# Performance work log

Measured on AMD Instinct MI355X. Metric: run time of the kernel, lower is better.

The kernel has to match this reference:

```python
import jax, jax.numpy as jnp
import numpy as np

N_RF = 25   # contour integration RF extent (must be odd, 7-55)
N_CH = 96   # AlexNet conv1 feature maps


def _get_coaligned_masks(weights_type, rf_len, non_overlapping_rfs=True):
    """Faithful numpy replication of the manually-defined coalignment masks."""
    half_rf = rf_len // 2
    kernel = np.zeros((N_CH, rf_len, rf_len), dtype=np.float32)
    step = 3 if non_overlapping_rfs else 1
    pre = list(range(0, half_rf, step))
    post = list(range(half_rf + step, rf_len, step))
    kernel[10, pre, half_rf] = 1
    kernel[10, post, half_rf] = 1
    if weights_type != 'enhance':
        kernel[10, half_rf, pre] = -1
        kernel[10, half_rf, post] = -1
    kernel[5, half_rf, pre] = 1
    kernel[5, half_rf, post] = 1
    if weights_type != 'enhance':
        kernel[5, pre, half_rf] = -1
        kernel[5, post, half_rf] = -1
    kernel[54, (1, 4, 6, 9, 15, 17, 20, 23), (8, 9, 10, 11, 13, 14, 15, 16)] = 1
    kernel[64, list(range(0, half_rf, 3)), list(range(0, half_rf, 3))] = 1
    kernel[64, list(range(half_rf + 3, rf_len, 3)), list(range(half_rf + 3, rf_len, 3))] = 1
    if weights_type != 'enhance':
        kernel[64, list(range(rf_len - 1, half_rf, -3)), list(range(0, half_rf, 3))] = -1
        kernel[64, list(range(half_rf - 3, -1, -3)), list(range(half_rf + 3, rf_len, 3))] = -1
    kernel[67, :, :] = np.copy(kernel[54, :, :])
    kernel[78, (1, 3, 7, 10, 14, 17, 21, 23), (17, 16, 14, 13, 11, 10, 8, 7)] = 1
    return kernel


def setup_inputs() -> dict:
    key = jax.random.key(0)
    x = jax.random.normal(key, (128, 55, 55, N_CH), dtype=jnp.float32)  # NHWC, AlexNet conv1 output
    kernel = jnp.asarray(_get_coaligned_masks('enhance_and_suppress', N_RF))  # [ch, n, n]
    return {"x": x, "kernel": kernel}


def reference(x, kernel):
    # The per-(i,j) python loop in the original is exactly a per-channel (depthwise)
    # cross-correlation with the fixed mask kernel, SAME padding (n//2 each side),
    # followed by (identity) activation and residual add.
    ch = x.shape[-1]
    k = jnp.transpose(kernel, (1, 2, 0))[:, :, None, :]  # [n, n, 1, ch] HWIO depthwise
    lateral = jax.lax.conv_general_dilated(
        x, k,
        window_strides=(1, 1),
        padding='SAME',
        dimension_numbers=('NHWC', 'HWIO', 'NHWC'),
        feature_group_count=ch,
    )
    # activation is linear (None) -> identity
    return lateral + x
```

## Files before the change

### kernel.cpp

```cpp
#include <hip/hip_runtime.h>

#define NCH   96
#define RF    25
#define HALF  12
#define HW    55
#define PLANE (HW * HW)
#define CAP   32
#define MAXA  4
#define NGRP  12

#define WS_META_OFF (NCH * 4 + NCH * CAP * 4 * 2)

__global__ __launch_bounds__(1024) void prep_all(
        const float* __restrict__ kern, int* __restrict__ counts,
        int* __restrict__ tap_off, float* __restrict__ tap_w,
        int* __restrict__ meta) {
    __shared__ int scnt[NCH];
    const int wave = threadIdx.x >> 6;
    const int lane = threadIdx.x & 63;
    for (int c = wave; c < NCH; c += 16) {
        const float* kc = kern + c * (RF * RF);
        int base = 0;
        for (int seg = 0; seg < RF * RF; seg += 64) {
            const int i = seg + lane;
            const float w = (i < RF * RF) ? kc[i] : 0.0f;
            const unsigned long long m = __ballot(w != 0.0f);
            const int pos = base + __popcll(m & ((1ull << lane) - 1ull));
            if (w != 0.0f && pos < CAP) {
                const int dy = i / RF, dx = i - dy * RF;
                tap_off[c * CAP + pos] = (dy << 8) | dx;
                tap_w[c * CAP + pos]   = w;
            }
            base += __popcll(m);
        }
        if (lane == 0) { counts[c] = base; scnt[c] = base; }
    }
    __syncthreads();
    if (threadIdx.x == 0) {
        int na[2] = {0, 0};
        bool fallback = false;
        for (int ch = 0; ch < NCH; ++ch) {
            if (scnt[ch] > 0) {
                if (scnt[ch] > CAP) fallback = true;
                const int h = ch / 48;
                if (na[h] < MAXA) meta[3 + h * MAXA + na[h]] = ch;
                ++na[h];
            }
        }
        if (na[0] > MAXA || na[1] > MAXA) fallback = true;
        meta[0] = fallback ? 999 : 0;
        meta[1] = na[0] < MAXA ? na[0] : MAXA;
        meta[2] = na[1] < MAXA ? na[1] : MAXA;
        for (int h = 0; h < 2; ++h)
            for (int i = na[h]; i < MAXA; ++i) meta[3 + h * MAXA + i] = 0;
    }
}

__global__ __launch_bounds__(1024, 4) void contour_img(
        const float* __restrict__ x, const float* __restrict__ kern,
        const int* __restrict__ counts, const int* __restrict__ tap_off,
        const float* __restrict__ tap_w, const int* __restrict__ meta,
        float* __restrict__ out) {
    __shared__ float sh[MAXA][HW][56];
    __shared__ float lat[MAXA * PLANE];
    __shared__ float tw[MAXA][CAP];
    __shared__ int   toff[MAXA][CAP];
    __shared__ int   tcnt[MAXA];
    __shared__ signed char c2l[48];
    __shared__ int   wrNow[NGRP];
    __shared__ int   dsec[3];
    __shared__ int   ndsS;

    const int tid = threadIdx.x;
    const int b   = blockIdx.x;
    const int n   = b >> 1;
    const int h   = b & 1;

    const float* xn = x   + (size_t)n * (PLANE * NCH);
    float*       on = out + (size_t)n * (PLANE * NCH);

    const bool fast = (meta[0] != 999);
    const int  na   = fast ? meta[1 + h] : 0;

    if (tid < 48) c2l[tid] = -1;
    __syncthreads();
    if (fast) {
        if (tid < na) {
            const int c = meta[3 + h * MAXA + tid];
            tcnt[tid] = counts[c];
            c2l[c - h * 48] = (signed char)tid;
        }
        if (tid >= 64 && tid < 64 + MAXA * CAP) {
            const int a = (tid - 64) / CAP, t = (tid - 64) % CAP;
            const int c = (a < na) ? meta[3 + h * MAXA + a] : h * 48;
            toff[a][t] = tap_off[c * CAP + t];
            tw[a][t]   = tap_w[c * CAP + t];
        }
    }
    __syncthreads();
    if (fast && tid == 0) {
        int nds = 0;
        for (int s = 0; s < 3; ++s) {
            bool act = false;
            for (int c = s * 16; c < s * 16 + 16; ++c) act |= (c2l[c] >= 0);
            for (int g = s * 4; g < s * 4 + 4; ++g) wrNow[g] = act ? 0 : 1;
            if (act) dsec[nds++] = s;
        }
        ndsS = nds;
    }
    __syncthreads();

    if (fast) {
        const float4* xs = (const float4*)xn;
        float4*       os = (float4*)on;
        const int base = h * NGRP;

        #pragma unroll 2
        for (int idx = tid; idx < PLANE * NGRP; idx += 1024) {
            const int px = idx / NGRP;
            const int gg = idx - px * NGRP;
            const int fi = px * 24 + base + gg;
            const float4 v = xs[fi];
            const int r = px / HW, col = px - r * HW;
            const int lc = gg * 4;
            const int a0 = c2l[lc + 0], a1 = c2l[lc + 1];
            const int a2 = c2l[lc + 2], a3 = c2l[lc + 3];
            if (a0 >= 0) sh[a0][r][col] = v.x;
            if (a1 >= 0) sh[a1][r][col] = v.y;
            if (a2 >= 0) sh[a2][r][col] = v.z;
            if (a3 >= 0) sh[a3][r][col] = v.w;
            if (wrNow[gg]) os[fi] = v;
        }
        __syncthreads();

        for (int idx = tid; idx < na * PLANE; idx += 1024) {
            const int a = idx / PLANE, p = idx - a * PLANE;
            const int r = p / HW, col = p - r * HW;
            const int cnt = tcnt[a];
            float acc = 0.0f;
            for (int t = 0; t < cnt; ++t) {
                const int off = toff[a][t];
                const float w = tw[a][t];
                const int yy = r   + (off >> 8)  - HALF;
                const int xx = col + (off & 255) - HALF;
                const bool ok = ((unsigned)yy < (unsigned)HW) &
                                ((unsigned)xx < (unsigned)HW);
                const int yc = min(max(yy, 0), HW - 1);
                const int xc = min(max(xx, 0), HW - 1);
                const float vv = sh[a][yc][xc];
                acc += ok ? w * vv : 0.0f;
            }
            lat[idx] = acc;
        }
        __syncthreads();

        const int nds  = ndsS;
        const int tot2 = PLANE * nds * 4;
        for (int idx = tid; idx < tot2; idx += 1024) {
            const int px  = idx / (nds * 4);
            const int rem = idx - px * (nds * 4);
            const int d = rem >> 2, j = rem & 3;
            const int gg = dsec[d] * 4 + j;
            const int fi = px * 24 + base + gg;
            float4 v = xs[fi];
            const int lc = gg * 4;
            const int a0 = c2l[lc + 0], a1 = c2l[lc + 1];
            const int a2 = c2l[lc + 2], a3 = c2l[lc + 3];
            if (a0 >= 0) v.x += lat[a0 * PLANE + px];
            if (a1 >= 0) v.y += lat[a1 * PLANE + px];
            if (a2 >= 0) v.z += lat[a2 * PLANE + px];
            if (a3 >= 0) v.w += lat[a3 * PLANE + px];
            os[fi] = v;
        }
    } else {
        const float4* xs = (const float4*)xn;
        float4*       os = (float4*)on;
        for (int idx = tid; idx < PLANE * NGRP; idx += 1024) {
            const int px = idx / NGRP;
            const int gg = idx - px * NGRP;
            const int r  = px / HW, col = px - r * HW;
            const int fi = px * 24 + h * NGRP + gg;
            const float4 xv = xs[fi];
            float acc[4] = {xv.x, xv.y, xv.z, xv.w};
            for (int kk = 0; kk < 4; ++kk) {
                const int c = h * 48 + gg * 4 + kk;
                const int cnt = counts[c];
                if (cnt == 0) continue;
                float aa = 0.0f;
                if (cnt <= CAP) {
                    for (int t = 0; t < cnt; ++t) {
                        const int off = tap_off[c * CAP + t];
                        const float w = tap_w[c * CAP + t];
                        const int dy = off >> 8, dx = off & 255;
                        const int yy = r   + dy - HALF;
                        const int xx = col + dx - HALF;
                        if ((unsigned)yy < (unsigned)HW &&
                            (unsigned)xx < (unsigned)HW)
                            aa += w * xn[(size_t)(yy * HW + xx) * NCH + c];
                    }
                } else {
                    for (int dy = 0; dy < RF; ++dy)
                        for (int dx = 0; dx < RF; ++dx) {
                            const float w = kern[(c * RF + dy) * RF + dx];
                            if (w == 0.0f) continue;
                            const int yy = r   + dy - HALF;
                            const int xx = col + dx - HALF;
                            if ((unsigned)yy < (unsigned)HW &&
                                (unsigned)xx < (unsigned)HW)
                                aa += w * xn[(size_t)(yy * HW + xx) * NCH + c];
                        }
                }
                acc[kk] += aa;
            }
            os[fi] = make_float4(acc[0], acc[1], acc[2], acc[3]);
        }
    }
}

extern "C" void kernel_launch(void* const* d_in, const int* in_sizes, int n_in,
                              void* d_out, int out_size, void* d_ws, size_t ws_size,
                              hipStream_t stream) {
    const float* x    = (const float*)d_in[0];
    const float* kern = (const float*)d_in[1];
    float* out = (float*)d_out;

    int*   counts  = (int*)d_ws;
    int*   tap_off = (int*)((char*)d_ws + NCH * 4);
    float* tap_w   = (float*)((char*)d_ws + NCH * 4 + NCH * CAP * 4);
    int*   meta    = (int*)((char*)d_ws + WS_META_OFF);

    prep_all<<<1, 1024, 0, stream>>>(kern, counts, tap_off, tap_w, meta);

    contour_img<<<256, 1024, 0, stream>>>(x, kern, counts, tap_off, tap_w, meta, out);
}
```

Measured before the change: 400.6 us.

## Split pass-through copy into separate blocks and fuse lateral conv with residual write

Launches 512 blocks: the first 256 handle only the 16-channel sections that contain active mask channels, and the extra 256 perform a grid-strided float4 copy of the inactive channel groups. The per-plane lateral result buffer in shared memory is removed, and the tap convolution is computed inline during the residual write, which cuts shared memory use and allows higher occupancy. The prep kernel now precomputes the active and inactive group lists. This trades a separate intermediate pass for a less regular thread mapping, where only 1024/ndg threads per group are on duty.

```diff
diff --git a/kernel.cpp b/kernel.cpp
--- a/kernel.cpp
+++ b/kernel.cpp
@@ -5,6 +5,7 @@
 #define HALF  12
 #define HW    55
 #define PLANE (HW * HW)
+#define NPIX  (128 * PLANE)
 #define CAP   32
 #define MAXA  4
 #define NGRP  12
@@ -52,39 +53,100 @@
         meta[1] = na[0] < MAXA ? na[0] : MAXA;
         meta[2] = na[1] < MAXA ? na[1] : MAXA;
         for (int h = 0; h < 2; ++h)
-            for (int i = na[h]; i < MAXA; ++i) meta[3 + h * MAXA + i] = 0;
-    }
-}
-
-__global__ __launch_bounds__(1024, 4) void contour_img(
+            for (int i = na[h] < MAXA ? na[h] : MAXA; i < MAXA; ++i)
+                meta[3 + h * MAXA + i] = 0;
+        int ngi = 0;
+        for (int h = 0; h < 2; ++h) {
+            int nd = 0;
+            for (int s = 0; s < 3; ++s) {
+                bool act = false;
+                for (int c = s * 16; c < s * 16 + 16; ++c)
+                    act |= (scnt[h * 48 + c] > 0);
+                if (act) { for (int g = s * 4; g < s * 4 + 4; ++g)
+                               meta[38 + h * 12 + nd++] = g; }
+                else     { for (int g = s * 4; g < s * 4 + 4; ++g)
+                               meta[12 + ngi++] = h * NGRP + g; }
+            }
+            meta[36 + h] = nd;
+        }
+        meta[11] = ngi;
+    }
+}
+
+__device__ __forceinline__ float conv_tap(const float (*shp)[56],
+        const int* __restrict__ toffA, const float* __restrict__ twA,
+        int cnt, int r, int col) {
+    float acc = 0.0f;
+    for (int t = 0; t < cnt; ++t) {
+        const int off = toffA[t];
+        const float w = twA[t];
+        const int yy = r   + (off >> 8)  - HALF;
+        const int xx = col + (off & 255) - HALF;
+        const bool ok = ((unsigned)yy < (unsigned)HW) &
+                        ((unsigned)xx < (unsigned)HW);
+        const int yc = min(max(yy, 0), HW - 1);
+        const int xc = min(max(xx, 0), HW - 1);
+        const float vv = shp[yc][xc];
+        acc += ok ? w * vv : 0.0f;
+    }
+    return acc;
+}
+
+__global__ __launch_bounds__(1024, 8) void contour_split(
         const float* __restrict__ x, const float* __restrict__ kern,
         const int* __restrict__ counts, const int* __restrict__ tap_off,
         const float* __restrict__ tap_w, const int* __restrict__ meta,
         float* __restrict__ out) {
     __shared__ float sh[MAXA][HW][56];
-    __shared__ float lat[MAXA * PLANE];
     __shared__ float tw[MAXA][CAP];
     __shared__ int   toff[MAXA][CAP];
     __shared__ int   tcnt[MAXA];
     __shared__ signed char c2l[48];
-    __shared__ int   wrNow[NGRP];
-    __shared__ int   dsec[3];
-    __shared__ int   ndsS;
+    __shared__ int   dgS[12];
+    __shared__ int   glS[24];
+    __shared__ int   ndgS, flagS;
 
     const int tid = threadIdx.x;
     const int b   = blockIdx.x;
-    const int n   = b >> 1;
-    const int h   = b & 1;
-
+
+    if (tid == 0) flagS = meta[0];
+    __syncthreads();
+    const bool fast = (flagS != 999);
+
+    if (b >= 256) {
+        if (!fast) return;
+        if (tid == 0) ndgS = meta[11];
+        if (tid < 24) glS[tid] = meta[12 + tid];
+        __syncthreads();
+        const int ngi = ndgS;
+        if (ngi == 0) return;
+        const int S    = 256 * 1024;
+        const int gt   = (b - 256) * 1024 + tid;
+        const int cols = S / ngi;
+        if (gt >= cols * ngi) return;
+        const int j = gt % ngi;
+        const int g = glS[j];
+        const float4* xs4 = (const float4*)x;
+        float4*       os4 = (float4*)out;
+        #pragma unroll 8
+        for (int p = gt / ngi; p < NPIX; p += cols) {
+            const int fi = p * 24 + g;
+            os4[fi] = xs4[fi];
+        }
+        return;
+    }
+
+    const int n = b >> 1;
+    const int h = b & 1;
     const float* xn = x   + (size_t)n * (PLANE * NCH);
     float*       on = out + (size_t)n * (PLANE * NCH);
 
-    const bool fast = (meta[0] != 999);
-    const int  na   = fast ? meta[1 + h] : 0;
-
-    if (tid < 48) c2l[tid] = -1;
-    __syncthreads();
     if (fast) {
+        const int na = meta[1 + h];
+        if (tid < 48) c2l[tid] = -1;
+        if (tid == 0) ndgS = meta[36 + h];
+        if (tid >= 128 && tid < 140) dgS[tid - 128] = meta[38 + h * 12 + (tid - 128)];
+        __syncthreads();
         if (tid < na) {
             const int c = meta[3 + h * MAXA + tid];
             tcnt[tid] = counts[c];
@@ -96,81 +158,55 @@
             toff[a][t] = tap_off[c * CAP + t];
             tw[a][t]   = tap_w[c * CAP + t];
         }
-    }
-    __syncthreads();
-    if (fast && tid == 0) {
-        int nds = 0;
-        for (int s = 0; s < 3; ++s) {
-            bool act = false;
-            for (int c = s * 16; c < s * 16 + 16; ++c) act |= (c2l[c] >= 0);
-            for (int g = s * 4; g < s * 4 + 4; ++g) wrNow[g] = act ? 0 : 1;
-            if (act) dsec[nds++] = s;
-        }
-        ndsS = nds;
-    }
-    __syncthreads();
-
-    if (fast) {
+        __syncthreads();
+
+        const int ndg = ndgS;
+        if (ndg == 0) return;
+        const int pstep = 1024 / ndg;
+        const bool on_duty = (tid < pstep * ndg);
+
+        int g = 0, a0 = -1, a1 = -1, a2 = -1, a3 = -1, pslot = 0;
+        if (on_duty) {
+            const int gslot = tid % ndg;
+            pslot = tid / ndg;
+            g = dgS[gslot];
+            const int lc = g * 4;
+            a0 = c2l[lc + 0]; a1 = c2l[lc + 1];
+            a2 = c2l[lc + 2]; a3 = c2l[lc + 3];
+        }
+        const int fbase = h * NGRP + g;
         const float4* xs = (const float4*)xn;
         float4*       os = (float4*)on;
-        const int base = h * NGRP;
-
-        #pragma unroll 2
-        for (int idx = tid; idx < PLANE * NGRP; idx += 1024) {
-            const int px = idx / NGRP;
-            const int gg = idx - px * NGRP;
-            const int fi = px * 24 + base + gg;
-            const float4 v = xs[fi];
-            const int r = px / HW, col = px - r * HW;
-            const int lc = gg * 4;
-            const int a0 = c2l[lc + 0], a1 = c2l[lc + 1];
-            const int a2 = c2l[lc + 2], a3 = c2l[lc + 3];
-            if (a0 >= 0) sh[a0][r][col] = v.x;
-            if (a1 >= 0) sh[a1][r][col] = v.y;
-            if (a2 >= 0) sh[a2][r][col] = v.z;
-            if (a3 >= 0) sh[a3][r][col] = v.w;
-            if (wrNow[gg]) os[fi] = v;
-        }
-        __syncthreads();
-
-        for (int idx = tid; idx < na * PLANE; idx += 1024) {
-            const int a = idx / PLANE, p = idx - a * PLANE;
-            const int r = p / HW, col = p - r * HW;
-            const int cnt = tcnt[a];
-            float acc = 0.0f;
-            for (int t = 0; t < cnt; ++t) {
-                const int off = toff[a][t];
-                const float w = tw[a][t];
-                const int yy = r   + (off >> 8)  - HALF;
-                const int xx = col + (off & 255) - HALF;
-                const bool ok = ((unsigned)yy < (unsigned)HW) &
-                                ((unsigned)xx < (unsigned)HW);
-                const int yc = min(max(yy, 0), HW - 1);
-                const int xc = min(max(xx, 0), HW - 1);
-                const float vv = sh[a][yc][xc];
-                acc += ok ? w * vv : 0.0f;
-            }
-            lat[idx] = acc;
-        }
-        __syncthreads();
-
-        const int nds  = ndsS;
-        const int tot2 = PLANE * nds * 4;
-        for (int idx = tid; idx < tot2; idx += 1024) {
-            const int px  = idx / (nds * 4);
-            const int rem = idx - px * (nds * 4);
-            const int d = rem >> 2, j = rem & 3;
-            const int gg = dsec[d] * 4 + j;
-            const int fi = px * 24 + base + gg;
-            float4 v = xs[fi];
-            const int lc = gg * 4;
-            const int a0 = c2l[lc + 0], a1 = c2l[lc + 1];
-            const int a2 = c2l[lc + 2], a3 = c2l[lc + 3];
-            if (a0 >= 0) v.x += lat[a0 * PLANE + px];
-            if (a1 >= 0) v.y += lat[a1 * PLANE + px];
-            if (a2 >= 0) v.z += lat[a2 * PLANE + px];
-            if (a3 >= 0) v.w += lat[a3 * PLANE + px];
-            os[fi] = v;
+
+        if (on_duty) {
+            #pragma unroll 4
+            for (int p = pslot; p < PLANE; p += pstep) {
+                const float4 v = xs[p * 24 + fbase];
+                const int r = p / HW, col = p - r * HW;
+                if (a0 >= 0) sh[a0][r][col] = v.x;
+                if (a1 >= 0) sh[a1][r][col] = v.y;
+                if (a2 >= 0) sh[a2][r][col] = v.z;
+                if (a3 >= 0) sh[a3][r][col] = v.w;
+            }
+        }
+        __syncthreads();
+
+        if (on_duty) {
+            const int cnt0 = (a0 >= 0) ? tcnt[a0] : 0;
+            const int cnt1 = (a1 >= 0) ? tcnt[a1] : 0;
+            const int cnt2 = (a2 >= 0) ? tcnt[a2] : 0;
+            const int cnt3 = (a3 >= 0) ? tcnt[a3] : 0;
+            #pragma unroll 2
+            for (int p = pslot; p < PLANE; p += pstep) {
+                const int fi = p * 24 + fbase;
+                float4 v = xs[fi];
+                const int r = p / HW, col = p - r * HW;
+                if (a0 >= 0) v.x += conv_tap(sh[a0], toff[a0], tw[a0], cnt0, r, col);
+                if (a1 >= 0) v.y += conv_tap(sh[a1], toff[a1], tw[a1], cnt1, r, col);
+                if (a2 >= 0) v.z += conv_tap(sh[a2], toff[a2], tw[a2], cnt2, r, col);
+                if (a3 >= 0) v.w += conv_tap(sh[a3], toff[a3], tw[a3], cnt3, r, col);
+                os[fi] = v;
+            }
         }
     } else {
         const float4* xs = (const float4*)xn;
@@ -191,9 +227,8 @@
                     for (int t = 0; t < cnt; ++t) {
                         const int off = tap_off[c * CAP + t];
                         const float w = tap_w[c * CAP + t];
-                        const int dy = off >> 8, dx = off & 255;
-                        const int yy = r   + dy - HALF;
-                        const int xx = col + dx - HALF;
+                        const int yy = r   + (off >> 8)  - HALF;
+                        const int xx = col + (off & 255) - HALF;
                         if ((unsigned)yy < (unsigned)HW &&
                             (unsigned)xx < (unsigned)HW)
                             aa += w * xn[(size_t)(yy * HW + xx) * NCH + c];
@@ -231,5 +266,5 @@
 
     prep_all<<<1, 1024, 0, stream>>>(kern, counts, tap_off, tap_w, meta);
 
-    contour_img<<<256, 1024, 0, stream>>>(x, kern, counts, tap_off, tap_w, meta, out);
-}
+    contour_split<<<512, 1024, 0, stream>>>(x, kern, counts, tap_off, tap_w, meta, out);
+}
```

Measured after the change: 415.7 us. 3.8% more time.
